# Performance work log

Measured on AMD Instinct MI355X. Metric: run time of the kernel, lower is better.

The kernel has to match this reference:

```python
import jax, jax.numpy as jnp
import numpy as np
from itertools import combinations

N = 128
D = 512
EPSILON = 32.0
VR_DIM = 2
SHARPNESS = 10.0


def _pairwise_dist(W):
    # [N, N] Euclidean distance matrix via GEMM
    sq = jnp.sum(W * W, axis=1)
    d2 = sq[:, None] + sq[None, :] - 2.0 * (W @ W.T)
    return jnp.sqrt(jnp.maximum(d2, 0.0))


def setup_inputs() -> dict:
    key = jax.random.key(0)
    W = jax.random.normal(key, (N, D), dtype=jnp.float32)
    return {"W": W}


def reference(W) -> jnp.ndarray:
    n = W.shape[0]
    dist = _pairwise_dist(W)  # [N, N]

    # 0-simplices: identity masks
    m0 = jnp.eye(n, dtype=W.dtype)

    # 1-simplices: soft sigmoid value at both endpoints of every pair
    iu, ju = np.triu_indices(n, k=1)  # static index arrays, P = C(N,2)
    P = iu.shape[0]
    d_pair = dist[iu, ju]
    # 1/(1+exp(s*(d-eps))) == sigmoid(s*(eps-d))
    val = jax.nn.sigmoid(SHARPNESS * (EPSILON - d_pair))
    rp = np.arange(P)
    m1 = jnp.zeros((P, n), dtype=W.dtype).at[rp, iu].set(val).at[rp, ju].set(val)

    parts = [m0, m1]

    if VR_DIM >= 2:
        # 2-simplices: hard indicator masks on all triples (zero row if not formed)
        tri = np.array(list(combinations(range(n), 3)), dtype=np.int32)  # [T, 3]
        ti, tj, tk = tri[:, 0], tri[:, 1], tri[:, 2]
        T = tri.shape[0]
        cond = (
            (dist[ti, tj] <= EPSILON)
            & (dist[tj, tk] <= EPSILON)
            & (dist[ti, tk] <= EPSILON)
        ).astype(W.dtype)
        rt = np.arange(T)
        m2 = (
            jnp.zeros((T, n), dtype=W.dtype)
            .at[rt, ti].set(cond)
            .at[rt, tj].set(cond)
            .at[rt, tk].set(cond)
        )
        parts.append(m2)

    return jnp.concatenate(parts, axis=0)
```

## Files before the change

kernel.cpp:

```cpp
#include <hip/hip_runtime.h>
#include <math.h>

#define NPTS     128
#define DIM      512
#define NPAIR    8128
#define NTRI     341376
#define ROW_PAIR0 128
#define ROW_TRI0  8256
#define NROWS    349632
#define FILL_BLOCKS 43704

__global__ void vr_dist_kernel(const float* __restrict__ W,
                               float* __restrict__ sigval,
                               unsigned long long* __restrict__ adj) {
    __shared__ float wi[DIM];
    const int i = blockIdx.x;
    const int j = threadIdx.x;
    for (int c = j; c < DIM; c += 128) wi[c] = W[i * DIM + c];
    __syncthreads();

    const float4* wj4 = (const float4*)(W + (size_t)j * DIM);
    const float4* wi4 = (const float4*)wi;
    double acc = 0.0;
    #pragma unroll 4
    for (int c = 0; c < DIM / 4; ++c) {
        float4 a = wi4[c];
        float4 b = wj4[c];
        double d0 = (double)a.x - (double)b.x;
        double d1 = (double)a.y - (double)b.y;
        double d2 = (double)a.z - (double)b.z;
        double d3 = (double)a.w - (double)b.w;
        acc = fma(d0, d0, acc);
        acc = fma(d1, d1, acc);
        acc = fma(d2, d2, acc);
        acc = fma(d3, d3, acc);
    }
    double dist = sqrt(acc);

    unsigned long long m = __ballot(dist <= 32.0);
    if ((j & 63) == 0) adj[i * 2 + (j >> 6)] = m;

    if (j > i) {
        int p = 127 * i - ((i * (i - 1)) >> 1) + (j - i - 1);
        float x = 10.0f * (32.0f - (float)dist);
        sigval[p] = 1.0f / (1.0f + expf(-x));
    }
}

__global__ __launch_bounds__(256) void vr_fill_kernel(
    const float* __restrict__ sigval,
    const unsigned long long* __restrict__ adj,
    float4* __restrict__ out) {
    __shared__ unsigned long long sadj[256];
    const int tid = threadIdx.x;
    sadj[tid] = adj[tid];
    __syncthreads();

    const int g   = blockIdx.x * 256 + tid;
    const int row = g >> 5;
    const int c0  = (g & 31) << 2;

    float4 v = make_float4(0.f, 0.f, 0.f, 0.f);
    float* vp = (float*)&v;

    if (row < ROW_PAIR0) {
        int d = row - c0;
        if (d >= 0 && d < 4) vp[d] = 1.0f;
    } else if (row < ROW_TRI0) {
        int p = row - ROW_PAIR0;
        int lo = 0, hi = 127;
        #pragma unroll
        for (int it = 0; it < 7; ++it) {
            int m = (lo + hi + 1) >> 1;
            int C = 127 * m - ((m * (m - 1)) >> 1);
            if (C <= p) lo = m; else hi = m - 1;
        }
        int i = lo;
        int j = i + 1 + (p - (127 * i - ((i * (i - 1)) >> 1)));
        float val = sigval[p];
        int di = i - c0, dj = j - c0;
        if (di >= 0 && di < 4) vp[di] = val;
        if (dj >= 0 && dj < 4) vp[dj] = val;
    } else {
        int t = row - ROW_TRI0;
        int lo = 0, hi = 125;
        #pragma unroll
        for (int it = 0; it < 7; ++it) {
            int m = (lo + hi + 1) >> 1;
            int rem = NPTS - m;
            int T = NTRI - rem * (rem - 1) * (rem - 2) / 6;
            if (T <= t) lo = m; else hi = m - 1;
        }
        int a = lo;
        int rema = NPTS - a;
        int r = t - (NTRI - rema * (rema - 1) * (rema - 2) / 6);
        lo = a + 1; hi = 126;
        #pragma unroll
        for (int it = 0; it < 7; ++it) {
            int m = (lo + hi + 1) >> 1;
            int C2 = ((m - a - 1) * (254 - a - m)) >> 1;
            if (C2 <= r) lo = m; else hi = m - 1;
        }
        int b = lo;
        int c = b + 1 + (r - (((b - a - 1) * (254 - a - b)) >> 1));

        unsigned long long bab = sadj[(a << 1) + (b >> 6)] >> (b & 63);
        unsigned long long bbc = sadj[(b << 1) + (c >> 6)] >> (c & 63);
        unsigned long long bac = sadj[(a << 1) + (c >> 6)] >> (c & 63);
        float cond = (float)(bab & bbc & bac & 1ull);

        int da = a - c0, db = b - c0, dc = c - c0;
        if (da >= 0 && da < 4) vp[da] = cond;
        if (db >= 0 && db < 4) vp[db] = cond;
        if (dc >= 0 && dc < 4) vp[dc] = cond;
    }
    out[g] = v;
}

extern "C" void kernel_launch(void* const* d_in, const int* in_sizes, int n_in,
                              void* d_out, int out_size, void* d_ws, size_t ws_size,
                              hipStream_t stream) {
    const float* W = (const float*)d_in[0];
    float* out = (float*)d_out;

    unsigned long long* adj = (unsigned long long*)d_ws;
    float* sigval = (float*)((char*)d_ws + 2048);

    vr_dist_kernel<<<128, 128, 0, stream>>>(W, sigval, adj);
    vr_fill_kernel<<<FILL_BLOCKS, 256, 0, stream>>>(sigval, adj, (float4*)out);
}
```

Before: 227.7 us.

## Decode each simplex row once per thread and stream rows with nontemporal stores

```diff
diff --git a/kernel.cpp b/kernel.cpp
--- a/kernel.cpp
+++ b/kernel.cpp
@@ -1,14 +1,16 @@
 #include <hip/hip_runtime.h>
 #include <math.h>
 
-#define NPTS     128
-#define DIM      512
-#define NPAIR    8128
-#define NTRI     341376
+#define NPTS      128
+#define DIM       512
+#define NPAIR     8128
+#define NTRI      341376
 #define ROW_PAIR0 128
 #define ROW_TRI0  8256
-#define NROWS    349632
-#define FILL_BLOCKS 43704
+#define NROWS     349632
+#define FILL_BLOCKS 1366
+
+typedef float vfloat4 __attribute__((ext_vector_type(4)));
 
 __global__ void vr_dist_kernel(const float* __restrict__ W,
                                float* __restrict__ sigval,
@@ -21,7 +23,7 @@
 
     const float4* wj4 = (const float4*)(W + (size_t)j * DIM);
     const float4* wi4 = (const float4*)wi;
-    double acc = 0.0;
+    double a0 = 0.0, a1 = 0.0, a2 = 0.0, a3 = 0.0;
     #pragma unroll 4
     for (int c = 0; c < DIM / 4; ++c) {
         float4 a = wi4[c];
@@ -30,12 +32,12 @@
         double d1 = (double)a.y - (double)b.y;
         double d2 = (double)a.z - (double)b.z;
         double d3 = (double)a.w - (double)b.w;
-        acc = fma(d0, d0, acc);
-        acc = fma(d1, d1, acc);
-        acc = fma(d2, d2, acc);
-        acc = fma(d3, d3, acc);
+        a0 = fma(d0, d0, a0);
+        a1 = fma(d1, d1, a1);
+        a2 = fma(d2, d2, a2);
+        a3 = fma(d3, d3, a3);
     }
-    double dist = sqrt(acc);
+    double dist = sqrt((a0 + a1) + (a2 + a3));
 
     unsigned long long m = __ballot(dist <= 32.0);
     if ((j & 63) == 0) adj[i * 2 + (j >> 6)] = m;
@@ -50,22 +52,23 @@
 __global__ __launch_bounds__(256) void vr_fill_kernel(
     const float* __restrict__ sigval,
     const unsigned long long* __restrict__ adj,
-    float4* __restrict__ out) {
+    vfloat4* __restrict__ out) {
     __shared__ unsigned long long sadj[256];
+    __shared__ int   spack[256];
+    __shared__ float sval[256];
+
     const int tid = threadIdx.x;
     sadj[tid] = adj[tid];
     __syncthreads();
 
-    const int g   = blockIdx.x * 256 + tid;
-    const int row = g >> 5;
-    const int c0  = (g & 31) << 2;
+    const int row0 = blockIdx.x * 256;
+    const int row  = row0 + tid;
 
-    float4 v = make_float4(0.f, 0.f, 0.f, 0.f);
-    float* vp = (float*)&v;
-
+    int   pack = 255 | (255 << 8) | (255 << 16);
+    float val  = 0.0f;
     if (row < ROW_PAIR0) {
-        int d = row - c0;
-        if (d >= 0 && d < 4) vp[d] = 1.0f;
+        pack = row | (255 << 8) | (255 << 16);
+        val  = 1.0f;
     } else if (row < ROW_TRI0) {
         int p = row - ROW_PAIR0;
         int lo = 0, hi = 127;
@@ -77,11 +80,9 @@
         }
         int i = lo;
         int j = i + 1 + (p - (127 * i - ((i * (i - 1)) >> 1)));
-        float val = sigval[p];
-        int di = i - c0, dj = j - c0;
-        if (di >= 0 && di < 4) vp[di] = val;
-        if (dj >= 0 && dj < 4) vp[dj] = val;
-    } else {
+        pack = i | (j << 8) | (255 << 16);
+        val  = sigval[p];
+    } else if (row < NROWS) {
         int t = row - ROW_TRI0;
         int lo = 0, hi = 125;
         #pragma unroll
@@ -107,14 +108,34 @@
         unsigned long long bab = sadj[(a << 1) + (b >> 6)] >> (b & 63);
         unsigned long long bbc = sadj[(b << 1) + (c >> 6)] >> (c & 63);
         unsigned long long bac = sadj[(a << 1) + (c >> 6)] >> (c & 63);
-        float cond = (float)(bab & bbc & bac & 1ull);
+        val  = (float)(bab & bbc & bac & 1ull);
+        pack = a | (b << 8) | (c << 16);
+    }
+    spack[tid] = pack;
+    sval[tid]  = val;
+    __syncthreads();
 
-        int da = a - c0, db = b - c0, dc = c - c0;
-        if (da >= 0 && da < 4) vp[da] = cond;
-        if (db >= 0 && db < 4) vp[db] = cond;
-        if (dc >= 0 && dc < 4) vp[dc] = cond;
+    const int col4 = tid & 31;
+    const int c0   = col4 << 2;
+    const int rsub = tid >> 5;
+
+    #pragma unroll 4
+    for (int k = 0; k < 32; ++k) {
+        int rl = (k << 3) + rsub;
+        int pk = spack[rl];
+        float vv = sval[rl];
+        int a = pk & 255, b = (pk >> 8) & 255, c = (pk >> 16) & 255;
+
+        vfloat4 v;
+        v.x = (a == c0     || b == c0     || c == c0    ) ? vv : 0.0f;
+        v.y = (a == c0 + 1 || b == c0 + 1 || c == c0 + 1) ? vv : 0.0f;
+        v.z = (a == c0 + 2 || b == c0 + 2 || c == c0 + 2) ? vv : 0.0f;
+        v.w = (a == c0 + 3 || b == c0 + 3 || c == c0 + 3) ? vv : 0.0f;
+
+        int grow = row0 + rl;
+        if (grow < NROWS)
+            __builtin_nontemporal_store(v, &out[(size_t)grow * 32 + col4]);
     }
-    out[g] = v;
 }
 
 extern "C" void kernel_launch(void* const* d_in, const int* in_sizes, int n_in,
@@ -127,5 +148,5 @@
     float* sigval = (float*)((char*)d_ws + 2048);
 
     vr_dist_kernel<<<128, 128, 0, stream>>>(W, sigval, adj);
-    vr_fill_kernel<<<FILL_BLOCKS, 256, 0, stream>>>(sigval, adj, (float4*)out);
+    vr_fill_kernel<<<FILL_BLOCKS, 256, 0, stream>>>(sigval, adj, (vfloat4*)out);
 }
```

Result: faster. 202.0 us (-11.3%).
